# Optimization experiments

Measured on AMD Instinct MI355X. Metric: run time of the kernel, lower is better.

## Reference

```python
import jax, jax.numpy as jnp
import numpy as np

N = 100000       # nodes
E = 1600000      # edges (avg degree 16)
F_IN, HID, C, K = 64, 64, 16, 3


def setup_inputs() -> dict:
    key = jax.random.key(0)
    ks = jax.random.split(key, 4)
    x = jax.random.normal(ks[0], (N, F_IN), dtype=jnp.float32)
    edge_index = jax.random.randint(ks[1], (2, E), 0, N, dtype=jnp.int32)
    s1 = 1.0 / np.sqrt(F_IN)
    W1 = jax.random.uniform(ks[2], (K, F_IN, HID), jnp.float32, -s1, s1)
    b1 = jnp.zeros((HID,), jnp.float32)
    s2 = 1.0 / np.sqrt(HID)
    W2 = jax.random.uniform(ks[3], (K, HID, C), jnp.float32, -s2, s2)
    b2 = jnp.zeros((C,), jnp.float32)
    return {"x": x, "edge_index": edge_index, "W1": W1, "b1": b1, "W2": W2, "b2": b2}


def _cheb_conv(x, row, col, wedge, W, b):
    """PyG ChebConv with sym norm, lambda_max=2: L_hat = -D^-1/2 A D^-1/2."""
    prop = lambda h: jax.ops.segment_sum(h[col] * wedge[:, None], row, num_segments=N)
    Tx0 = x
    out = Tx0 @ W[0]
    Tx1 = prop(x)
    out = out + Tx1 @ W[1]
    for k in range(2, W.shape[0]):
        Tx2 = 2.0 * prop(Tx1) - Tx0
        out = out + Tx2 @ W[k]
        Tx0, Tx1 = Tx1, Tx2
    return out + b


def reference(x, edge_index, W1, b1, W2, b2):
    row, col = edge_index[0], edge_index[1]
    deg = jax.ops.segment_sum(jnp.ones((edge_index.shape[1],), x.dtype), row, num_segments=N)
    dinv = jnp.where(deg > 0, jax.lax.rsqrt(jnp.maximum(deg, 1.0)), 0.0)
    wedge = -dinv[row] * dinv[col]  # scaled-Laplacian edge weights
    h = jax.nn.relu(_cheb_conv(x, row, col, wedge, W1, b1))
    # dropout: identity in eval mode
    out = _cheb_conv(h, row, col, wedge, W2, b2)
    return jax.nn.log_softmax(out, axis=1)
```

## Files before the change

### kernel.cpp

```cpp
#include <hip/hip_runtime.h>

#define NN 100000
#define NE 1600000
#define NBUCK 196
#define CAP 10240

typedef __attribute__((ext_vector_type(8))) short bf16x8;
typedef __attribute__((ext_vector_type(4))) short bf16x4;
typedef __attribute__((ext_vector_type(4))) float f32x4;

__device__ inline unsigned short f2bf(float f) {
    unsigned int u = __float_as_uint(f);
    return (unsigned short)((u + 0x7FFFu + ((u >> 16) & 1u)) >> 16);
}
__device__ inline float bf2f(short s) {
    return __uint_as_float(((unsigned int)(unsigned short)s) << 16);
}

__global__ __launch_bounds__(256) void k_bin(const int* __restrict__ row, const int* __restrict__ col,
                                             int* __restrict__ gcursor, int* __restrict__ ebuf) {
    __shared__ int hist[NBUCK];
    for (int i = threadIdx.x; i < NBUCK; i += 256) hist[i] = 0;
    __syncthreads();
    int start = blockIdx.x * 6250;
    int end = start + 6250; if (end > NE) end = NE;
    for (int e = start + threadIdx.x; e < end; e += 256)
        atomicAdd(&hist[row[e] >> 9], 1);
    __syncthreads();
    for (int i = threadIdx.x; i < NBUCK; i += 256)
        hist[i] = atomicAdd(&gcursor[i], hist[i]);
    __syncthreads();
    for (int e = start + threadIdx.x; e < end; e += 256) {
        int r = row[e], c = col[e];
        int bk = r >> 9;
        int pos = atomicAdd(&hist[bk], 1);
        if (pos < CAP) ebuf[bk * CAP + pos] = (c << 9) | (r & 511);
    }
}

__global__ void k_bstart(const int* __restrict__ gcursor, int* __restrict__ bstart,
                         int* __restrict__ row_ptr) {
    __shared__ int s[256];
    int t = threadIdx.x;
    int d = (t < NBUCK) ? gcursor[t] : 0;
    s[t] = d; __syncthreads();
    for (int off = 1; off < 256; off <<= 1) {
        int v = (t >= off) ? s[t - off] : 0;
        __syncthreads();
        s[t] += v;
        __syncthreads();
    }
    if (t < NBUCK) bstart[t] = s[t] - d;
    if (t == NBUCK - 1) bstart[NBUCK] = s[t];
    if (t == 0) row_ptr[NN] = NE;
}

__global__ __launch_bounds__(256) void k_build(const int* __restrict__ ebuf, const int* __restrict__ bstart,
                                               int* __restrict__ row_ptr, float* __restrict__ dinv,
                                               int* __restrict__ col_sorted) {
    __shared__ int deg[512], cur[512], ps[256];
    int b = blockIdx.x;
    int bs = bstart[b], cnt = bstart[b + 1] - bs;
    const int* eb = ebuf + (size_t)b * CAP;
    int t = threadIdx.x;
    deg[t] = 0; deg[t + 256] = 0;
    __syncthreads();
    for (int e = t; e < cnt; e += 256)
        atomicAdd(&deg[eb[e] & 511], 1);
    __syncthreads();
    int d0 = deg[2 * t], d1 = deg[2 * t + 1];
    int p = d0 + d1;
    ps[t] = p; __syncthreads();
    for (int off = 1; off < 256; off <<= 1) {
        int v = (t >= off) ? ps[t - off] : 0;
        __syncthreads();
        ps[t] += v;
        __syncthreads();
    }
    int base = bs + ps[t] - p;
    cur[2 * t] = base; cur[2 * t + 1] = base + d0;
    int n0 = (b << 9) + 2 * t, n1 = n0 + 1;
    if (n0 < NN) { row_ptr[n0] = base;      dinv[n0] = d0 > 0 ? rsqrtf((float)d0) : 0.f; }
    if (n1 < NN) { row_ptr[n1] = base + d0; dinv[n1] = d1 > 0 ? rsqrtf((float)d1) : 0.f; }
    __syncthreads();
    for (int e = t; e < cnt; e += 256) {
        int w = eb[e];
        int pos = atomicAdd(&cur[w & 511], 1);
        col_sorted[pos] = ((unsigned)w) >> 9;
    }
}

__global__ void k_scale(const float* __restrict__ x, const float* __restrict__ dinv,
                        unsigned short* __restrict__ xsbf, unsigned short* __restrict__ xbf) {
    int t = blockIdx.x * 256 + threadIdx.x;
    if (t < NN * 16) {
        float d = dinv[t >> 4];
        float4 v = ((const float4*)x)[t];
        bf16x4 u, s;
        u[0] = (short)f2bf(v.x); u[1] = (short)f2bf(v.y); u[2] = (short)f2bf(v.z); u[3] = (short)f2bf(v.w);
        s[0] = (short)f2bf(v.x * d); s[1] = (short)f2bf(v.y * d); s[2] = (short)f2bf(v.z * d); s[3] = (short)f2bf(v.w * d);
        ((bf16x4*)xbf)[t] = u;
        ((bf16x4*)xsbf)[t] = s;
    }
}

__global__ __launch_bounds__(256) void k_spmm64b(const unsigned short* __restrict__ ins,
                                                 const unsigned short* __restrict__ subbf,
                                                 unsigned short* __restrict__ outb,
                                                 unsigned short* __restrict__ outsb,
                                                 const int* __restrict__ row_ptr, const int* __restrict__ cs,
                                                 const float* __restrict__ dinv,
                                                 int has_sub, int has_outs) {
    int n = blockIdx.x * 4 + (threadIdx.x >> 6);
    if (n >= NN) return;
    int nu = __builtin_amdgcn_readfirstlane(n);
    int lane = threadIdx.x & 63;
    int es = lane >> 3;
    int f = lane & 7;
    int s = row_ptr[nu], e = row_ptr[nu + 1];
    float a0[8] = {0,0,0,0,0,0,0,0}, a1[8] = {0,0,0,0,0,0,0,0};
    int i = s;
    for (; i + 15 < e; i += 16) {
        int c0 = cs[i + es];
        int c1 = cs[i + 8 + es];
        bf16x8 v0 = *((const bf16x8*)(ins + (size_t)c0 * 64 + f * 8));
        bf16x8 v1 = *((const bf16x8*)(ins + (size_t)c1 * 64 + f * 8));
        #pragma unroll
        for (int j = 0; j < 8; ++j) { a0[j] += bf2f(v0[j]); a1[j] += bf2f(v1[j]); }
    }
    for (; i + 7 < e; i += 8) {
        int c0 = cs[i + es];
        bf16x8 v0 = *((const bf16x8*)(ins + (size_t)c0 * 64 + f * 8));
        #pragma unroll
        for (int j = 0; j < 8; ++j) a0[j] += bf2f(v0[j]);
    }
    if (i + es < e) {
        int c0 = cs[i + es];
        bf16x8 v0 = *((const bf16x8*)(ins + (size_t)c0 * 64 + f * 8));
        #pragma unroll
        for (int j = 0; j < 8; ++j) a0[j] += bf2f(v0[j]);
    }
    float a[8];
    #pragma unroll
    for (int j = 0; j < 8; ++j) {
        a[j] = a0[j] + a1[j];
        a[j] += __shfl_xor(a[j], 8);
        a[j] += __shfl_xor(a[j], 16);
        a[j] += __shfl_xor(a[j], 32);
    }
    if (es == 0) {
        float dn = dinv[nu];
        float r[8];
        #pragma unroll
        for (int j = 0; j < 8; ++j) r[j] = -dn * a[j];
        if (has_sub) {
            bf16x8 sv = *((const bf16x8*)(subbf + (size_t)nu * 64 + f * 8));
            #pragma unroll
            for (int j = 0; j < 8; ++j) r[j] = 2.f * r[j] - bf2f(sv[j]);
        }
        bf16x8 ob;
        #pragma unroll
        for (int j = 0; j < 8; ++j) ob[j] = (short)f2bf(r[j]);
        *((bf16x8*)(outb + (size_t)nu * 64 + f * 8)) = ob;
        if (has_outs) {
            bf16x8 os;
            #pragma unroll
            for (int j = 0; j < 8; ++j) os[j] = (short)f2bf(dn * r[j]);
            *((bf16x8*)(outsb + (size_t)nu * 64 + f * 8)) = os;
        }
    }
}

__global__ __launch_bounds__(256) void k_dense1(const unsigned short* __restrict__ xbf,
                                                const unsigned short* __restrict__ t1bf,
                                                const unsigned short* __restrict__ t2bf,
                                                const float* __restrict__ W,
                                                const float* __restrict__ b,
                                                unsigned short* __restrict__ hbf) {
    __shared__ unsigned short Wf[24 * 64 * 8];
    for (int slot = threadIdx.x; slot < 24 * 64; slot += 256) {
        int c = slot / 384;
        int t = (slot / 64) % 6;
        int l = slot & 63;
        int rr = l & 15, gg = l >> 4;
        unsigned int pk[4];
        #pragma unroll
        for (int jp = 0; jp < 4; ++jp) {
            int k0 = t * 32 + gg * 8 + jp * 2;
            unsigned int lo = f2bf(W[(k0 >> 6) * 4096 + (k0 & 63) * 64 + c * 16 + rr]);
            int k1 = k0 + 1;
            unsigned int hi = f2bf(W[(k1 >> 6) * 4096 + (k1 & 63) * 64 + c * 16 + rr]);
            pk[jp] = lo | (hi << 16);
        }
        *((uint4*)&Wf[slot * 8]) = *((uint4*)pk);
    }
    __syncthreads();

    int lane = threadIdx.x & 63;
    int r = lane & 15, g = lane >> 4;
    bf16x8 bfr[4][6];
    #pragma unroll
    for (int c = 0; c < 4; ++c)
        #pragma unroll
        for (int t = 0; t < 6; ++t)
            bfr[c][t] = *((const bf16x8*)&Wf[((c * 6 + t) * 64 + lane) * 8]);

    float bl[4];
    #pragma unroll
    for (int c = 0; c < 4; ++c) bl[c] = b[c * 16 + r];

    const unsigned short* arrs[3] = {xbf, t1bf, t2bf};
    int wid = blockIdx.x * 4 + (threadIdx.x >> 6);
    int wstride = gridDim.x * 4;
    for (int tile = wid; tile < NN / 16; tile += wstride) {
        int nb = tile * 16;
        bf16x8 af[6];
        #pragma unroll
        for (int t = 0; t < 6; ++t)
            af[t] = *((const bf16x8*)(arrs[t >> 1] + (size_t)(nb + r) * 64 + (t & 1) * 32 + g * 8));
        f32x4 acc[4];
        #pragma unroll
        for (int c = 0; c < 4; ++c) acc[c] = (f32x4){bl[c], bl[c], bl[c], bl[c]};
        #pragma unroll
        for (int t = 0; t < 6; ++t)
            #pragma unroll
            for (int c = 0; c < 4; ++c)
                acc[c] = __builtin_amdgcn_mfma_f32_16x16x32_bf16(af[t], bfr[c][t], acc[c], 0, 0, 0);
        #pragma unroll
        for (int c = 0; c < 4; ++c)
            #pragma unroll
            for (int q = 0; q < 4; ++q)
                hbf[(size_t)(nb + g * 4 + q) * 64 + c * 16 + r] = f2bf(fmaxf(acc[c][q], 0.f));
    }
}

__global__ __launch_bounds__(256) void k_proj(const unsigned short* __restrict__ hbf,
                                              const float* __restrict__ W2,
                                              const float* __restrict__ b2, const float* __restrict__ dinv,
                                              float* __restrict__ Apre, unsigned short* __restrict__ Gsb) {
    __shared__ unsigned short Wf[6 * 64 * 8];
    for (int slot = threadIdx.x; slot < 6 * 64; slot += 256) {
        int c = slot / 128;
        int t = (slot / 64) & 1;
        int l = slot & 63;
        int rr = l & 15, gg = l >> 4;
        unsigned int pk[4];
        #pragma unroll
        for (int jp = 0; jp < 4; ++jp) {
            int k0 = t * 32 + gg * 8 + jp * 2;
            int k1 = k0 + 1;
            float w0, w1;
            if (c == 0)      { w0 = W2[k0 * 16 + rr] - W2[2048 + k0 * 16 + rr];
                               w1 = W2[k1 * 16 + rr] - W2[2048 + k1 * 16 + rr]; }
            else if (c == 1) { w0 = W2[1024 + k0 * 16 + rr]; w1 = W2[1024 + k1 * 16 + rr]; }
            else             { w0 = W2[2048 + k0 * 16 + rr]; w1 = W2[2048 + k1 * 16 + rr]; }
            pk[jp] = (unsigned int)f2bf(w0) | ((unsigned int)f2bf(w1) << 16);
        }
        *((uint4*)&Wf[slot * 8]) = *((uint4*)pk);
    }
    __syncthreads();

    int lane = threadIdx.x & 63;
    int r = lane & 15, g = lane >> 4;
    bf16x8 bfr[3][2];
    #pragma unroll
    for (int c = 0; c < 3; ++c)
        #pragma unroll
        for (int t = 0; t < 2; ++t)
            bfr[c][t] = *((const bf16x8*)&Wf[((c * 2 + t) * 64 + lane) * 8]);
    float b2r = b2[r];

    int wid = blockIdx.x * 4 + (threadIdx.x >> 6);
    int wstride = gridDim.x * 4;
    for (int tile = wid; tile < NN / 16; tile += wstride) {
        int nb = tile * 16;
        bf16x8 af[2];
        #pragma unroll
        for (int t = 0; t < 2; ++t)
            af[t] = *((const bf16x8*)(hbf + (size_t)(nb + r) * 64 + t * 32 + g * 8));
        f32x4 acc[3];
        #pragma unroll
        for (int c = 0; c < 3; ++c) acc[c] = (f32x4){0.f, 0.f, 0.f, 0.f};
        #pragma unroll
        for (int t = 0; t < 2; ++t)
            #pragma unroll
            for (int c = 0; c < 3; ++c)
                acc[c] = __builtin_amdgcn_mfma_f32_16x16x32_bf16(af[t], bfr[c][t], acc[c], 0, 0, 0);
        #pragma unroll
        for (int q = 0; q < 4; ++q) {
            int n = nb + g * 4 + q;
            float dv = dinv[n];
            Apre[(size_t)n * 16 + r] = acc[0][q] + b2r;
            Gsb[(size_t)n * 32 + r]      = f2bf(acc[1][q] * dv);
            Gsb[(size_t)n * 32 + 16 + r] = f2bf(acc[2][q] * dv);
        }
    }
}

__global__ __launch_bounds__(256) void k_spmm32b(const unsigned short* __restrict__ Gsb,
                                                 float* __restrict__ q1, unsigned short* __restrict__ tsb,
                                                 const int* __restrict__ row_ptr, const int* __restrict__ cs,
                                                 const float* __restrict__ dinv) {
    int n = blockIdx.x * 4 + (threadIdx.x >> 6);
    if (n >= NN) return;
    int nu = __builtin_amdgcn_readfirstlane(n);
    int lane = threadIdx.x & 63;
    int es = lane >> 3;
    int f = lane & 7;
    int s = row_ptr[nu], e = row_ptr[nu + 1];
    float a0[4] = {0,0,0,0}, a1[4] = {0,0,0,0};
    int i = s;
    for (; i + 15 < e; i += 16) {
        int c0 = cs[i + es];
        int c1 = cs[i + 8 + es];
        bf16x4 v0 = *((const bf16x4*)(Gsb + (size_t)c0 * 32 + f * 4));
        bf16x4 v1 = *((const bf16x4*)(Gsb + (size_t)c1 * 32 + f * 4));
        #pragma unroll
        for (int j = 0; j < 4; ++j) { a0[j] += bf2f(v0[j]); a1[j] += bf2f(v1[j]); }
    }
    for (; i + 7 < e; i += 8) {
        int c0 = cs[i + es];
        bf16x4 v0 = *((const bf16x4*)(Gsb + (size_t)c0 * 32 + f * 4));
        #pragma unroll
        for (int j = 0; j < 4; ++j) a0[j] += bf2f(v0[j]);
    }
    if (i + es < e) {
        int c0 = cs[i + es];
        bf16x4 v0 = *((const bf16x4*)(Gsb + (size_t)c0 * 32 + f * 4));
        #pragma unroll
        for (int j = 0; j < 4; ++j) a0[j] += bf2f(v0[j]);
    }
    float a[4];
    #pragma unroll
    for (int j = 0; j < 4; ++j) {
        a[j] = a0[j] + a1[j];
        a[j] += __shfl_xor(a[j], 8);
        a[j] += __shfl_xor(a[j], 16);
        a[j] += __shfl_xor(a[j], 32);
    }
    if (es == 0) {
        float dn = dinv[nu];
        if (f < 4) {
            float4 w;
            w.x = -dn * a[0]; w.y = -dn * a[1]; w.z = -dn * a[2]; w.w = -dn * a[3];
            *((float4*)(q1 + (size_t)nu * 16 + f * 4)) = w;
        } else {
            bf16x4 w;
            #pragma unroll
            for (int j = 0; j < 4; ++j) w[j] = (short)f2bf(dn * (-dn * a[j]));
            *((bf16x4*)(tsb + (size_t)nu * 16 + (f - 4) * 4)) = w;
        }
    }
}

__global__ __launch_bounds__(256) void k_spmm16f(const unsigned short* __restrict__ tsb,
                                                 const float* __restrict__ Apre, const float* __restrict__ q1,
                                                 const int* __restrict__ row_ptr, const int* __restrict__ cs,
                                                 const float* __restrict__ dinv, float* __restrict__ out) {
    int n = blockIdx.x * 4 + (threadIdx.x >> 6);
    if (n >= NN) return;
    int nu = __builtin_amdgcn_readfirstlane(n);
    int lane = threadIdx.x & 63;
    int es = lane >> 2;
    int f = lane & 3;
    int s = row_ptr[nu], e = row_ptr[nu + 1];
    float a0[4] = {0,0,0,0}, a1[4] = {0,0,0,0};
    int i = s;
    for (; i + 31 < e; i += 32) {
        int c0 = cs[i + es];
        int c1 = cs[i + 16 + es];
        bf16x4 v0 = *((const bf16x4*)(tsb + (size_t)c0 * 16 + f * 4));
        bf16x4 v1 = *((const bf16x4*)(tsb + (size_t)c1 * 16 + f * 4));
        #pragma unroll
        for (int j = 0; j < 4; ++j) { a0[j] += bf2f(v0[j]); a1[j] += bf2f(v1[j]); }
    }
    for (; i + 15 < e; i += 16) {
        int c0 = cs[i + es];
        bf16x4 v0 = *((const bf16x4*)(tsb + (size_t)c0 * 16 + f * 4));
        #pragma unroll
        for (int j = 0; j < 4; ++j) a0[j] += bf2f(v0[j]);
    }
    if (i + es < e) {
        int c0 = cs[i + es];
        bf16x4 v0 = *((const bf16x4*)(tsb + (size_t)c0 * 16 + f * 4));
        #pragma unroll
        for (int j = 0; j < 4; ++j) a0[j] += bf2f(v0[j]);
    }
    float a[4];
    #pragma unroll
    for (int j = 0; j < 4; ++j) {
        a[j] = a0[j] + a1[j];
        a[j] += __shfl_xor(a[j], 4);
        a[j] += __shfl_xor(a[j], 8);
        a[j] += __shfl_xor(a[j], 16);
        a[j] += __shfl_xor(a[j], 32);
    }
    if (es == 0) {
        float dn = dinv[nu];
        float o[4];
        #pragma unroll
        for (int j = 0; j < 4; ++j)
            o[j] = Apre[(size_t)nu * 16 + f * 4 + j] + q1[(size_t)nu * 16 + f * 4 + j]
                   + 2.f * (-dn * a[j]);
        float m = fmaxf(fmaxf(o[0], o[1]), fmaxf(o[2], o[3]));
        m = fmaxf(m, __shfl_xor(m, 1));
        m = fmaxf(m, __shfl_xor(m, 2));
        float ssum = expf(o[0] - m) + expf(o[1] - m) + expf(o[2] - m) + expf(o[3] - m);
        ssum += __shfl_xor(ssum, 1);
        ssum += __shfl_xor(ssum, 2);
        float ls = logf(ssum);
        float4 w;
        w.x = o[0] - m - ls; w.y = o[1] - m - ls; w.z = o[2] - m - ls; w.w = o[3] - m - ls;
        *((float4*)(out + (size_t)nu * 16 + f * 4)) = w;
    }
}

extern "C" void kernel_launch(void* const* d_in, const int* in_sizes, int n_in,
                              void* d_out, int out_size, void* d_ws, size_t ws_size,
                              hipStream_t stream) {
    const float* x  = (const float*)d_in[0];
    const int*   ei = (const int*)d_in[1];
    const int*   row = ei;
    const int*   col = ei + NE;
    const float* W1 = (const float*)d_in[2];
    const float* b1 = (const float*)d_in[3];
    const float* W2 = (const float*)d_in[4];
    const float* b2 = (const float*)d_in[5];
    float* out = (float*)d_out;

    char* base = (char*)d_ws;
    size_t off = 0;
    auto alloc = [&](size_t bytes) -> char* {
        char* r = base + off;
        off = (off + bytes + 255) & ~(size_t)255;
        return r;
    };
    int*   gcursor    = (int*)alloc(NBUCK * 4);
    int*   bstart     = (int*)alloc((NBUCK + 1) * 4);
    float* dinv       = (float*)alloc((size_t)NN * 4);
    int*   row_ptr    = (int*)alloc((size_t)(NN + 1) * 4);
    int*   ebuf       = (int*)alloc((size_t)NBUCK * CAP * 4);
    int*   col_sorted = (int*)alloc((size_t)NE * 4);
    unsigned short* Xbf  = (unsigned short*)alloc((size_t)NN * 64 * 2);
    unsigned short* XSbf = (unsigned short*)alloc((size_t)NN * 64 * 2);
    unsigned short* T1bf = (unsigned short*)alloc((size_t)NN * 64 * 2);
    unsigned short* T1s  = (unsigned short*)alloc((size_t)NN * 64 * 2);
    unsigned short* T2bf = (unsigned short*)alloc((size_t)NN * 64 * 2);
    unsigned short* Hbf  = (unsigned short*)alloc((size_t)NN * 64 * 2);
    float* Apre          = (float*)alloc((size_t)NN * 16 * 4);
    unsigned short* Gsb  = (unsigned short*)alloc((size_t)NN * 32 * 2);
    float* q1            = (float*)alloc((size_t)NN * 16 * 4);
    unsigned short* tsb  = (unsigned short*)alloc((size_t)NN * 16 * 2);

    hipMemsetAsync(gcursor, 0, NBUCK * 4, stream);

    k_bin<<<256, 256, 0, stream>>>(row, col, gcursor, ebuf);
    k_bstart<<<1, 256, 0, stream>>>(gcursor, bstart, row_ptr);
    k_build<<<NBUCK, 256, 0, stream>>>(ebuf, bstart, row_ptr, dinv, col_sorted);
    k_scale<<<(NN * 16 + 255) / 256, 256, 0, stream>>>(x, dinv, XSbf, Xbf);

    int nbS = (NN + 3) / 4;
    k_spmm64b<<<nbS, 256, 0, stream>>>(XSbf, nullptr, T1bf, T1s, row_ptr, col_sorted, dinv, 0, 1);
    k_spmm64b<<<nbS, 256, 0, stream>>>(T1s, Xbf, T2bf, nullptr, row_ptr, col_sorted, dinv, 1, 0);
    k_dense1<<<521, 256, 0, stream>>>(Xbf, T1bf, T2bf, W1, b1, Hbf);
    k_proj<<<521, 256, 0, stream>>>(Hbf, W2, b2, dinv, Apre, Gsb);
    k_spmm32b<<<nbS, 256, 0, stream>>>(Gsb, q1, tsb, row_ptr, col_sorted, dinv);
    k_spmm16f<<<nbS, 256, 0, stream>>>(tsb, Apre, q1, row_ptr, col_sorted, dinv, out);
}
```

Before: 244.4 us.

## Fuse scale into build and dense layer-1 with projection via LDS

Folds the bf16 conversion and degree scaling of x into the CSR build kernel, using per-block dinv held in shared memory. The first dense layer and the second-layer projection become one kernel that stages the ReLU hidden tile in a swizzled per-wave LDS buffer, so the hidden matrix no longer goes to global memory and back. SpMM tail loops are merged into a single guarded loop. This removes two launches and an intermediate round trip, at the cost of a build kernel with only 196 blocks doing the conversion and higher LDS use in the fused dense kernel.

```diff
diff --git a/kernel.cpp b/kernel.cpp
--- a/kernel.cpp
+++ b/kernel.cpp
@@ -56,9 +56,13 @@
 }
 
 __global__ __launch_bounds__(256) void k_build(const int* __restrict__ ebuf, const int* __restrict__ bstart,
+                                               const float* __restrict__ x,
                                                int* __restrict__ row_ptr, float* __restrict__ dinv,
-                                               int* __restrict__ col_sorted) {
+                                               int* __restrict__ col_sorted,
+                                               unsigned short* __restrict__ xsbf,
+                                               unsigned short* __restrict__ xbf) {
     __shared__ int deg[512], cur[512], ps[256];
+    __shared__ float sdinv[512];
     int b = blockIdx.x;
     int bs = bstart[b], cnt = bstart[b + 1] - bs;
     const int* eb = ebuf + (size_t)b * CAP;
@@ -79,28 +83,33 @@
     }
     int base = bs + ps[t] - p;
     cur[2 * t] = base; cur[2 * t + 1] = base + d0;
+    float di0 = d0 > 0 ? rsqrtf((float)d0) : 0.f;
+    float di1 = d1 > 0 ? rsqrtf((float)d1) : 0.f;
+    sdinv[2 * t] = di0; sdinv[2 * t + 1] = di1;
     int n0 = (b << 9) + 2 * t, n1 = n0 + 1;
-    if (n0 < NN) { row_ptr[n0] = base;      dinv[n0] = d0 > 0 ? rsqrtf((float)d0) : 0.f; }
-    if (n1 < NN) { row_ptr[n1] = base + d0; dinv[n1] = d1 > 0 ? rsqrtf((float)d1) : 0.f; }
+    if (n0 < NN) { row_ptr[n0] = base;      dinv[n0] = di0; }
+    if (n1 < NN) { row_ptr[n1] = base + d0; dinv[n1] = di1; }
     __syncthreads();
     for (int e = t; e < cnt; e += 256) {
         int w = eb[e];
         int pos = atomicAdd(&cur[w & 511], 1);
         col_sorted[pos] = ((unsigned)w) >> 9;
     }
-}
-
-__global__ void k_scale(const float* __restrict__ x, const float* __restrict__ dinv,
-                        unsigned short* __restrict__ xsbf, unsigned short* __restrict__ xbf) {
-    int t = blockIdx.x * 256 + threadIdx.x;
-    if (t < NN * 16) {
-        float d = dinv[t >> 4];
-        float4 v = ((const float4*)x)[t];
-        bf16x4 u, s;
-        u[0] = (short)f2bf(v.x); u[1] = (short)f2bf(v.y); u[2] = (short)f2bf(v.z); u[3] = (short)f2bf(v.w);
-        s[0] = (short)f2bf(v.x * d); s[1] = (short)f2bf(v.y * d); s[2] = (short)f2bf(v.z * d); s[3] = (short)f2bf(v.w * d);
-        ((bf16x4*)xbf)[t] = u;
-        ((bf16x4*)xsbf)[t] = s;
+    int nodeBase = b << 9;
+    for (int idx = t; idx < 512 * 16; idx += 256) {
+        int ln = idx >> 4;
+        int n = nodeBase + ln;
+        if (n < NN) {
+            float d = sdinv[ln];
+            size_t gi = (size_t)n * 16 + (idx & 15);
+            float4 v = ((const float4*)x)[gi];
+            bf16x4 u, sc;
+            u[0] = (short)f2bf(v.x); u[1] = (short)f2bf(v.y); u[2] = (short)f2bf(v.z); u[3] = (short)f2bf(v.w);
+            sc[0] = (short)f2bf(v.x * d); sc[1] = (short)f2bf(v.y * d);
+            sc[2] = (short)f2bf(v.z * d); sc[3] = (short)f2bf(v.w * d);
+            ((bf16x4*)xbf)[gi] = u;
+            ((bf16x4*)xsbf)[gi] = sc;
+        }
     }
 }
 
@@ -128,13 +137,7 @@
         #pragma unroll
         for (int j = 0; j < 8; ++j) { a0[j] += bf2f(v0[j]); a1[j] += bf2f(v1[j]); }
     }
-    for (; i + 7 < e; i += 8) {
-        int c0 = cs[i + es];
-        bf16x8 v0 = *((const bf16x8*)(ins + (size_t)c0 * 64 + f * 8));
-        #pragma unroll
-        for (int j = 0; j < 8; ++j) a0[j] += bf2f(v0[j]);
-    }
-    if (i + es < e) {
+    for (; i + es < e; i += 8) {
         int c0 = cs[i + es];
         bf16x8 v0 = *((const bf16x8*)(ins + (size_t)c0 * 64 + f * 8));
         #pragma unroll
@@ -171,13 +174,16 @@
     }
 }
 
-__global__ __launch_bounds__(256) void k_dense1(const unsigned short* __restrict__ xbf,
-                                                const unsigned short* __restrict__ t1bf,
-                                                const unsigned short* __restrict__ t2bf,
-                                                const float* __restrict__ W,
-                                                const float* __restrict__ b,
-                                                unsigned short* __restrict__ hbf) {
-    __shared__ unsigned short Wf[24 * 64 * 8];
+__global__ __launch_bounds__(256) void k_d1p(const unsigned short* __restrict__ xbf,
+                                             const unsigned short* __restrict__ t1bf,
+                                             const unsigned short* __restrict__ t2bf,
+                                             const float* __restrict__ W1, const float* __restrict__ b1,
+                                             const float* __restrict__ W2, const float* __restrict__ b2,
+                                             const float* __restrict__ dinv,
+                                             float* __restrict__ Apre, unsigned short* __restrict__ Gsb) {
+    __shared__ unsigned short Wf1[24 * 64 * 8];
+    __shared__ unsigned short Wf2[6 * 64 * 8];
+    __shared__ unsigned short Ht[4][1024];
     for (int slot = threadIdx.x; slot < 24 * 64; slot += 256) {
         int c = slot / 384;
         int t = (slot / 64) % 6;
@@ -187,58 +193,13 @@
         #pragma unroll
         for (int jp = 0; jp < 4; ++jp) {
             int k0 = t * 32 + gg * 8 + jp * 2;
-            unsigned int lo = f2bf(W[(k0 >> 6) * 4096 + (k0 & 63) * 64 + c * 16 + rr]);
+            unsigned int lo = f2bf(W1[(k0 >> 6) * 4096 + (k0 & 63) * 64 + c * 16 + rr]);
             int k1 = k0 + 1;
-            unsigned int hi = f2bf(W[(k1 >> 6) * 4096 + (k1 & 63) * 64 + c * 16 + rr]);
+            unsigned int hi = f2bf(W1[(k1 >> 6) * 4096 + (k1 & 63) * 64 + c * 16 + rr]);
             pk[jp] = lo | (hi << 16);
         }
-        *((uint4*)&Wf[slot * 8]) = *((uint4*)pk);
-    }
-    __syncthreads();
-
-    int lane = threadIdx.x & 63;
-    int r = lane & 15, g = lane >> 4;
-    bf16x8 bfr[4][6];
-    #pragma unroll
-    for (int c = 0; c < 4; ++c)
-        #pragma unroll
-        for (int t = 0; t < 6; ++t)
-            bfr[c][t] = *((const bf16x8*)&Wf[((c * 6 + t) * 64 + lane) * 8]);
-
-    float bl[4];
-    #pragma unroll
-    for (int c = 0; c < 4; ++c) bl[c] = b[c * 16 + r];
-
-    const unsigned short* arrs[3] = {xbf, t1bf, t2bf};
-    int wid = blockIdx.x * 4 + (threadIdx.x >> 6);
-    int wstride = gridDim.x * 4;
-    for (int tile = wid; tile < NN / 16; tile += wstride) {
-        int nb = tile * 16;
-        bf16x8 af[6];
-        #pragma unroll
-        for (int t = 0; t < 6; ++t)
-            af[t] = *((const bf16x8*)(arrs[t >> 1] + (size_t)(nb + r) * 64 + (t & 1) * 32 + g * 8));
-        f32x4 acc[4];
-        #pragma unroll
-        for (int c = 0; c < 4; ++c) acc[c] = (f32x4){bl[c], bl[c], bl[c], bl[c]};
-        #pragma unroll
-        for (int t = 0; t < 6; ++t)
-            #pragma unroll
-            for (int c = 0; c < 4; ++c)
-                acc[c] = __builtin_amdgcn_mfma_f32_16x16x32_bf16(af[t], bfr[c][t], acc[c], 0, 0, 0);
-        #pragma unroll
-        for (int c = 0; c < 4; ++c)
-            #pragma unroll
-            for (int q = 0; q < 4; ++q)
-                hbf[(size_t)(nb + g * 4 + q) * 64 + c * 16 + r] = f2bf(fmaxf(acc[c][q], 0.f));
-    }
-}
-
-__global__ __launch_bounds__(256) void k_proj(const unsigned short* __restrict__ hbf,
-                                              const float* __restrict__ W2,
-                                              const float* __restrict__ b2, const float* __restrict__ dinv,
-                                              float* __restrict__ Apre, unsigned short* __restrict__ Gsb) {
-    __shared__ unsigned short Wf[6 * 64 * 8];
+        *((uint4*)&Wf1[slot * 8]) = *((uint4*)pk);
+    }
     for (int slot = threadIdx.x; slot < 6 * 64; slot += 256) {
         int c = slot / 128;
         int t = (slot / 64) & 1;
@@ -256,43 +217,81 @@
             else             { w0 = W2[2048 + k0 * 16 + rr]; w1 = W2[2048 + k1 * 16 + rr]; }
             pk[jp] = (unsigned int)f2bf(w0) | ((unsigned int)f2bf(w1) << 16);
         }
-        *((uint4*)&Wf[slot * 8]) = *((uint4*)pk);
+        *((uint4*)&Wf2[slot * 8]) = *((uint4*)pk);
     }
     __syncthreads();
 
     int lane = threadIdx.x & 63;
     int r = lane & 15, g = lane >> 4;
-    bf16x8 bfr[3][2];
+    int widx = threadIdx.x >> 6;
+    char* ht = (char*)Ht[widx];
+
+    bf16x8 bfr1[4][6];
+    #pragma unroll
+    for (int c = 0; c < 4; ++c)
+        #pragma unroll
+        for (int t = 0; t < 6; ++t)
+            bfr1[c][t] = *((const bf16x8*)&Wf1[((c * 6 + t) * 64 + lane) * 8]);
+    bf16x8 bfr2[3][2];
     #pragma unroll
     for (int c = 0; c < 3; ++c)
         #pragma unroll
         for (int t = 0; t < 2; ++t)
-            bfr[c][t] = *((const bf16x8*)&Wf[((c * 2 + t) * 64 + lane) * 8]);
+            bfr2[c][t] = *((const bf16x8*)&Wf2[((c * 2 + t) * 64 + lane) * 8]);
+
+    float bl[4];
+    #pragma unroll
+    for (int c = 0; c < 4; ++c) bl[c] = b1[c * 16 + r];
     float b2r = b2[r];
 
-    int wid = blockIdx.x * 4 + (threadIdx.x >> 6);
+    const unsigned short* arrs[3] = {xbf, t1bf, t2bf};
+    int wid = blockIdx.x * 4 + widx;
     int wstride = gridDim.x * 4;
     for (int tile = wid; tile < NN / 16; tile += wstride) {
         int nb = tile * 16;
-        bf16x8 af[2];
+        bf16x8 af[6];
+        #pragma unroll
+        for (int t = 0; t < 6; ++t)
+            af[t] = *((const bf16x8*)(arrs[t >> 1] + (size_t)(nb + r) * 64 + (t & 1) * 32 + g * 8));
+        f32x4 acc[4];
+        #pragma unroll
+        for (int c = 0; c < 4; ++c) acc[c] = (f32x4){bl[c], bl[c], bl[c], bl[c]};
+        #pragma unroll
+        for (int t = 0; t < 6; ++t)
+            #pragma unroll
+            for (int c = 0; c < 4; ++c)
+                acc[c] = __builtin_amdgcn_mfma_f32_16x16x32_bf16(af[t], bfr1[c][t], acc[c], 0, 0, 0);
+        #pragma unroll
+        for (int c = 0; c < 4; ++c)
+            #pragma unroll
+            for (int q = 0; q < 4; ++q) {
+                int node = g * 4 + q;
+                int byte = (node * 64 + c * 16 + r) * 2;
+                byte ^= (node & 7) << 4;
+                *((unsigned short*)(ht + byte)) = f2bf(fmaxf(acc[c][q], 0.f));
+            }
+        bf16x8 af2[2];
+        #pragma unroll
+        for (int t = 0; t < 2; ++t) {
+            int byte = (r * 64 + t * 32 + g * 8) * 2;
+            byte ^= (r & 7) << 4;
+            af2[t] = *((const bf16x8*)(ht + byte));
+        }
+        f32x4 acc2[3];
+        #pragma unroll
+        for (int c = 0; c < 3; ++c) acc2[c] = (f32x4){0.f, 0.f, 0.f, 0.f};
         #pragma unroll
         for (int t = 0; t < 2; ++t)
-            af[t] = *((const bf16x8*)(hbf + (size_t)(nb + r) * 64 + t * 32 + g * 8));
-        f32x4 acc[3];
-        #pragma unroll
-        for (int c = 0; c < 3; ++c) acc[c] = (f32x4){0.f, 0.f, 0.f, 0.f};
-        #pragma unroll
-        for (int t = 0; t < 2; ++t)
             #pragma unroll
             for (int c = 0; c < 3; ++c)
-                acc[c] = __builtin_amdgcn_mfma_f32_16x16x32_bf16(af[t], bfr[c][t], acc[c], 0, 0, 0);
+                acc2[c] = __builtin_amdgcn_mfma_f32_16x16x32_bf16(af2[t], bfr2[c][t], acc2[c], 0, 0, 0);
         #pragma unroll
         for (int q = 0; q < 4; ++q) {
             int n = nb + g * 4 + q;
             float dv = dinv[n];
-            Apre[(size_t)n * 16 + r] = acc[0][q] + b2r;
-            Gsb[(size_t)n * 32 + r]      = f2bf(acc[1][q] * dv);
-            Gsb[(size_t)n * 32 + 16 + r] = f2bf(acc[2][q] * dv);
+            Apre[(size_t)n * 16 + r] = acc2[0][q] + b2r;
+            Gsb[(size_t)n * 32 + r]      = f2bf(acc2[1][q] * dv);
+            Gsb[(size_t)n * 32 + 16 + r] = f2bf(acc2[2][q] * dv);
         }
     }
 }
@@ -318,13 +317,7 @@
         #pragma unroll
         for (int j = 0; j < 4; ++j) { a0[j] += bf2f(v0[j]); a1[j] += bf2f(v1[j]); }
     }
-    for (; i + 7 < e; i += 8) {
-        int c0 = cs[i + es];
-        bf16x4 v0 = *((const bf16x4*)(Gsb + (size_t)c0 * 32 + f * 4));
-        #pragma unroll
-        for (int j = 0; j < 4; ++j) a0[j] += bf2f(v0[j]);
-    }
-    if (i + es < e) {
+    for (; i + es < e; i += 8) {
         int c0 = cs[i + es];
         bf16x4 v0 = *((const bf16x4*)(Gsb + (size_t)c0 * 32 + f * 4));
         #pragma unroll
@@ -374,13 +367,7 @@
         #pragma unroll
         for (int j = 0; j < 4; ++j) { a0[j] += bf2f(v0[j]); a1[j] += bf2f(v1[j]); }
     }
-    for (; i + 15 < e; i += 16) {
-        int c0 = cs[i + es];
-        bf16x4 v0 = *((const bf16x4*)(tsb + (size_t)c0 * 16 + f * 4));
-        #pragma unroll
-        for (int j = 0; j < 4; ++j) a0[j] += bf2f(v0[j]);
-    }
-    if (i + es < e) {
+    for (; i + es < e; i += 16) {
         int c0 = cs[i + es];
         bf16x4 v0 = *((const bf16x4*)(tsb + (size_t)c0 * 16 + f * 4));
         #pragma unroll
@@ -446,7 +433,6 @@
     unsigned short* T1bf = (unsigned short*)alloc((size_t)NN * 64 * 2);
     unsigned short* T1s  = (unsigned short*)alloc((size_t)NN * 64 * 2);
     unsigned short* T2bf = (unsigned short*)alloc((size_t)NN * 64 * 2);
-    unsigned short* Hbf  = (unsigned short*)alloc((size_t)NN * 64 * 2);
     float* Apre          = (float*)alloc((size_t)NN * 16 * 4);
     unsigned short* Gsb  = (unsigned short*)alloc((size_t)NN * 32 * 2);
     float* q1            = (float*)alloc((size_t)NN * 16 * 4);
@@ -456,14 +442,12 @@
 
     k_bin<<<256, 256, 0, stream>>>(row, col, gcursor, ebuf);
     k_bstart<<<1, 256, 0, stream>>>(gcursor, bstart, row_ptr);
-    k_build<<<NBUCK, 256, 0, stream>>>(ebuf, bstart, row_ptr, dinv, col_sorted);
-    k_scale<<<(NN * 16 + 255) / 256, 256, 0, stream>>>(x, dinv, XSbf, Xbf);
+    k_build<<<NBUCK, 256, 0, stream>>>(ebuf, bstart, x, row_ptr, dinv, col_sorted, XSbf, Xbf);
 
     int nbS = (NN + 3) / 4;
     k_spmm64b<<<nbS, 256, 0, stream>>>(XSbf, nullptr, T1bf, T1s, row_ptr, col_sorted, dinv, 0, 1);
     k_spmm64b<<<nbS, 256, 0, stream>>>(T1s, Xbf, T2bf, nullptr, row_ptr, col_sorted, dinv, 1, 0);
-    k_dense1<<<521, 256, 0, stream>>>(Xbf, T1bf, T2bf, W1, b1, Hbf);
-    k_proj<<<521, 256, 0, stream>>>(Hbf, W2, b2, dinv, Apre, Gsb);
+    k_d1p<<<625, 256, 0, stream>>>(Xbf, T1bf, T2bf, W1, b1, W2, b2, dinv, Apre, Gsb);
     k_spmm32b<<<nbS, 256, 0, stream>>>(Gsb, q1, tsb, row_ptr, col_sorted, dinv);
     k_spmm16f<<<nbS, 256, 0, stream>>>(tsb, Apre, q1, row_ptr, col_sorted, dinv, out);
 }
```

New measurement: 244.8 us. About the same (+0.1%).
